# Optimization experiments

Measured on AMD Instinct MI355X. Metric: run time of the kernel, lower is better.

Reference implementation:

```python
import jax, jax.numpy as jnp
import numpy as np


def setup_inputs() -> dict:
    key = jax.random.key(0)
    k1, k2, k3 = jax.random.split(key, 3)
    B, S, D = 8, 2048, 1024
    lstm_output = jax.random.normal(k1, (B, S, D), dtype=jnp.float32)
    W = jax.random.normal(k2, (D, D), dtype=jnp.float32) * (1.0 / np.sqrt(D))
    b = jax.random.normal(k3, (D,), dtype=jnp.float32) * 0.01
    return {"lstm_output": lstm_output, "W": W, "b": b}


def reference(lstm_output, W, b):
    # proj(x) = x @ W^T + b  (torch nn.Linear convention: W is [out, in])
    proj = jnp.einsum('bsd,ed->bse', lstm_output, W) + b          # [B,S,D]
    # scores[b,i,j] = x[b,i] . proj[b,j]
    attn_scores = jnp.einsum('bid,bjd->bij', lstm_output, proj)   # [B,S,S]
    attn_weights = jax.nn.softmax(attn_scores, axis=-1)           # [B,S,S]
    context_vector = jnp.einsum('bij,bjd->bid', attn_weights, lstm_output)
    return (context_vector, attn_weights)
```

## Files before the change

### kernel.cpp

```cpp
#include <hip/hip_runtime.h>


typedef _Float16 f16;
typedef _Float16 f16x8 __attribute__((ext_vector_type(8)));
typedef _Float16 f16x4 __attribute__((ext_vector_type(4)));
typedef float f32x4 __attribute__((ext_vector_type(4)));
typedef unsigned int u32;

#define AS1 __attribute__((address_space(1)))
#define AS3 __attribute__((address_space(3)))

static constexpr int Bb = 8, Ss = 2048, Dd = 1024;

__global__ __launch_bounds__(256) void split_cast_k(
    const float* __restrict__ in, f16* __restrict__ hi, f16* __restrict__ lo,
    size_t n4) {
  size_t i = (size_t)blockIdx.x * 256 + threadIdx.x;
  if (i >= n4) return;
  float4 v = ((const float4*)in)[i];
  f16x4 h, l;
  h[0] = (f16)v.x; l[0] = (f16)(v.x - (float)h[0]);
  h[1] = (f16)v.y; l[1] = (f16)(v.y - (float)h[1]);
  h[2] = (f16)v.z; l[2] = (f16)(v.z - (float)h[2]);
  h[3] = (f16)v.w; l[3] = (f16)(v.w - (float)h[3]);
  ((f16x4*)hi)[i] = h;
  ((f16x4*)lo)[i] = l;
}

__global__ __launch_bounds__(256) void cast_k(const float* __restrict__ in,
                                              f16* __restrict__ out,
                                              size_t n4) {
  size_t i = (size_t)blockIdx.x * 256 + threadIdx.x;
  if (i >= n4) return;
  float4 v = ((const float4*)in)[i];
  f16x4 h;
  h[0] = (f16)v.x; h[1] = (f16)v.y; h[2] = (f16)v.z; h[3] = (f16)v.w;
  ((f16x4*)out)[i] = h;
}

__global__ __launch_bounds__(256) void transpose_cast_k(
    const float* __restrict__ x, f16* __restrict__ xT) {
  __shared__ f16 tile[32][33];
  const int b = blockIdx.z;
  const int s0 = blockIdx.x * 32, d0 = blockIdx.y * 32;
  const int tx = threadIdx.x & 31, ty = threadIdx.x >> 5;
  const float* xb = x + (size_t)b * Ss * Dd;
#pragma unroll
  for (int r = 0; r < 32; r += 8)
    tile[ty + r][tx] = (f16)xb[(size_t)(s0 + ty + r) * Dd + d0 + tx];
  __syncthreads();
  f16* xTb = xT + (size_t)b * Dd * Ss;
#pragma unroll
  for (int r = 0; r < 32; r += 8)
    xTb[(size_t)(d0 + ty + r) * Ss + s0 + tx] = tile[tx][ty + r];
}

template <int PPW>
__device__ __forceinline__ void stage_tile(const f16* __restrict__ g,
                                           size_t ld, f16* lds, int wave,
                                           int lane) {
#pragma unroll
  for (int c = 0; c < PPW; ++c) {
    int panel = wave * PPW + c;
    const f16* gp =
        g + (size_t)(panel * 16 + (lane & 15)) * ld + (lane >> 4) * 8;
    AS3 u32* lp = (AS3 u32*)(lds + panel * 512);
    __builtin_amdgcn_global_load_lds((const AS1 u32*)gp, lp, 16, 0, 0);
  }
}

template <bool DUAL_A, bool OUT_F16>
__global__ __launch_bounds__(256, 2) void gemm_bt(
    const f16* __restrict__ A0, const f16* __restrict__ A1,
    const f16* __restrict__ B0, float* __restrict__ C, f16* __restrict__ Ch,
    const float* __restrict__ bias, int K, size_t ldc, size_t sA, size_t sB,
    size_t sC) {
  const int tid = threadIdx.x;
  const int wave = tid >> 6, lane = tid & 63;
  const size_t tn = (size_t)blockIdx.x * 256;
  const size_t tm = (size_t)blockIdx.y * 128;
  const int b = blockIdx.z;

  constexpr int STAGE = (DUAL_A ? 4 : 3) * 4096;
  constexpr int BOFF = DUAL_A ? 8192 : 4096;
  __shared__ f16 smem[2 * STAGE];

  const f16* Ah = A0 + (size_t)b * sA + tm * (size_t)K;
  const f16* Al = DUAL_A ? (A1 + (size_t)b * sA + tm * (size_t)K) : nullptr;
  const f16* Bp = B0 + (size_t)b * sB + tn * (size_t)K;

  const int pA = (wave >> 1) * 4;
  const int pB = (wave & 1) * 8;

  auto stage_all = [&](int k, f16* buf) {
    stage_tile<2>(Ah + k, K, buf, wave, lane);
    if constexpr (DUAL_A) stage_tile<2>(Al + k, K, buf + 4096, wave, lane);
    stage_tile<4>(Bp + k, K, buf + BOFF, wave, lane);
  };

  f32x4 acc[4][8] = {};

  stage_all(0, smem);
  const int nIter = K / 32;
  for (int it = 0; it < nIter; ++it) {
    f16* cur = smem + (it & 1) * STAGE;
    f16* nxt = smem + ((it + 1) & 1) * STAGE;
    __syncthreads();
    if (it + 1 < nIter) stage_all((it + 1) * 32, nxt);
    f16x8 ah[4], al[4];
#pragma unroll
    for (int i = 0; i < 4; ++i) {
      ah[i] = *(const f16x8*)&cur[(pA + i) * 512 + lane * 8];
      if constexpr (DUAL_A)
        al[i] = *(const f16x8*)&cur[4096 + (pA + i) * 512 + lane * 8];
    }
#pragma unroll
    for (int j = 0; j < 8; ++j) {
      f16x8 bf = *(const f16x8*)&cur[BOFF + (pB + j) * 512 + lane * 8];
#pragma unroll
      for (int i = 0; i < 4; ++i) {
        acc[i][j] =
            __builtin_amdgcn_mfma_f32_16x16x32_f16(ah[i], bf, acc[i][j], 0, 0, 0);
        if constexpr (DUAL_A)
          acc[i][j] = __builtin_amdgcn_mfma_f32_16x16x32_f16(al[i], bf,
                                                             acc[i][j], 0, 0, 0);
      }
    }
  }

  const int wm = pA * 16, wn = pB * 16;
#pragma unroll
  for (int i = 0; i < 4; ++i) {
    size_t row0 = tm + wm + i * 16 + ((lane >> 4) << 2);
#pragma unroll
    for (int j = 0; j < 8; ++j) {
      size_t col = tn + wn + j * 16 + (lane & 15);
      float bj = bias ? bias[col] : 0.f;
#pragma unroll
      for (int r = 0; r < 4; ++r) {
        float v = acc[i][j][r] + bj;
        size_t off = (size_t)b * sC + (row0 + r) * ldc + col;
        if constexpr (OUT_F16)
          Ch[off] = (f16)v;
        else
          C[off] = v;
      }
    }
  }
}

__global__ __launch_bounds__(256) void softmax_k(float* __restrict__ sc,
                                                 f16* __restrict__ wh) {
  const size_t row = blockIdx.x;
  float* p = sc + row * 2048;
  f16* w = wh + row * 2048;
  const int t = threadIdx.x;
  float4 v0 = ((const float4*)p)[t];
  float4 v1 = ((const float4*)p)[256 + t];
  float m = fmaxf(fmaxf(fmaxf(v0.x, v0.y), fmaxf(v0.z, v0.w)),
                  fmaxf(fmaxf(v1.x, v1.y), fmaxf(v1.z, v1.w)));
#pragma unroll
  for (int o = 32; o; o >>= 1) m = fmaxf(m, __shfl_xor(m, o, 64));
  __shared__ float red[4];
  if ((t & 63) == 0) red[t >> 6] = m;
  __syncthreads();
  m = fmaxf(fmaxf(red[0], red[1]), fmaxf(red[2], red[3]));
  v0.x = __expf(v0.x - m);
  v0.y = __expf(v0.y - m);
  v0.z = __expf(v0.z - m);
  v0.w = __expf(v0.w - m);
  v1.x = __expf(v1.x - m);
  v1.y = __expf(v1.y - m);
  v1.z = __expf(v1.z - m);
  v1.w = __expf(v1.w - m);
  float s = v0.x + v0.y + v0.z + v0.w + v1.x + v1.y + v1.z + v1.w;
#pragma unroll
  for (int o = 32; o; o >>= 1) s += __shfl_xor(s, o, 64);
  __shared__ float red2[4];
  if ((t & 63) == 0) red2[t >> 6] = s;
  __syncthreads();
  s = red2[0] + red2[1] + red2[2] + red2[3];
  float inv = 1.0f / s;
  v0.x *= inv; v0.y *= inv; v0.z *= inv; v0.w *= inv;
  v1.x *= inv; v1.y *= inv; v1.z *= inv; v1.w *= inv;
  ((float4*)p)[t] = v0;
  ((float4*)p)[256 + t] = v1;
  f16x4 h0, h1;
  h0[0] = (f16)v0.x; h0[1] = (f16)v0.y; h0[2] = (f16)v0.z; h0[3] = (f16)v0.w;
  h1[0] = (f16)v1.x; h1[1] = (f16)v1.y; h1[2] = (f16)v1.z; h1[3] = (f16)v1.w;
  ((f16x4*)w)[t] = h0;
  ((f16x4*)w)[256 + t] = h1;
}

extern "C" void kernel_launch(void* const* d_in, const int* in_sizes, int n_in,
                              void* d_out, int out_size, void* d_ws,
                              size_t ws_size, hipStream_t stream) {
  (void)in_sizes; (void)n_in; (void)out_size; (void)ws_size;
  const float* x = (const float*)d_in[0];
  const float* W = (const float*)d_in[1];
  const float* bias = (const float*)d_in[2];
  float* ctx = (float*)d_out;
  float* scores = (float*)d_out + (size_t)Bb * Ss * Dd;

  const size_t nBSD = (size_t)Bb * Ss * Dd;
  const size_t nDD = (size_t)Dd * Dd;

  f16* p = (f16*)d_ws;
  f16* x_hi = p; p += nBSD;
  f16* x_lo = p; p += nBSD;
  f16* xT   = p; p += nBSD;
  f16* W_hi = p; p += nDD;
  f16* p_hi = p; p += nBSD;
  f16* attnw = x_hi;

  split_cast_k<<<(unsigned)(nBSD / 4 / 256), 256, 0, stream>>>(x, x_hi, x_lo,
                                                               nBSD / 4);
  cast_k<<<(unsigned)(nDD / 4 / 256), 256, 0, stream>>>(W, W_hi, nDD / 4);
  transpose_cast_k<<<dim3(Ss / 32, Dd / 32, Bb), 256, 0, stream>>>(x, xT);

  gemm_bt<true, true><<<dim3(Dd / 256, (Bb * Ss) / 128, 1), 256, 0, stream>>>(
      x_hi, x_lo, W_hi, nullptr, p_hi, bias, Dd, (size_t)Dd, 0, 0, 0);

  gemm_bt<true, false><<<dim3(Ss / 256, Ss / 128, Bb), 256, 0, stream>>>(
      x_hi, x_lo, p_hi, scores, nullptr, nullptr, Dd, (size_t)Ss,
      (size_t)Ss * Dd, (size_t)Ss * Dd, (size_t)Ss * Ss);

  softmax_k<<<Bb * Ss, 256, 0, stream>>>(scores, attnw);

  gemm_bt<false, false><<<dim3(Dd / 256, Ss / 128, Bb), 256, 0, stream>>>(
      attnw, nullptr, xT, ctx, nullptr, nullptr, Ss, (size_t)Dd,
      (size_t)Ss * Ss, (size_t)Dd * Ss, (size_t)Ss * Dd);
}
```

Measured before the change: 631.2 us.

## Enlarge GEMM tiles to 256x256 with 8 waves and triple-buffered LDS pipeline

The GEMM kernel now runs 512 threads on a 256x256 output tile. A three-stage LDS ring is filled asynchronously, and explicit vmcnt waits let loads run two iterations ahead while only a single barrier is used per iteration. MFMA sections are wrapped in raised wave priority. The aim is to improve reuse and hide global load latency, at the cost of large dynamic LDS (up to 144KB), which limits occupancy to one block per CU and may leave fewer blocks to fill the machine.

```diff
diff --git a/kernel.cpp b/kernel.cpp
--- a/kernel.cpp
+++ b/kernel.cpp
@@ -70,53 +70,68 @@
 }
 
 template <bool DUAL_A, bool OUT_F16>
-__global__ __launch_bounds__(256, 2) void gemm_bt(
+__global__ __launch_bounds__(512, 2) void gemm_bt(
     const f16* __restrict__ A0, const f16* __restrict__ A1,
     const f16* __restrict__ B0, float* __restrict__ C, f16* __restrict__ Ch,
     const float* __restrict__ bias, int K, size_t ldc, size_t sA, size_t sB,
     size_t sC) {
+  extern __shared__ f16 smem[];
   const int tid = threadIdx.x;
   const int wave = tid >> 6, lane = tid & 63;
   const size_t tn = (size_t)blockIdx.x * 256;
-  const size_t tm = (size_t)blockIdx.y * 128;
+  const size_t tm = (size_t)blockIdx.y * 256;
   const int b = blockIdx.z;
 
-  constexpr int STAGE = (DUAL_A ? 4 : 3) * 4096;
-  constexpr int BOFF = DUAL_A ? 8192 : 4096;
-  __shared__ f16 smem[2 * STAGE];
+  constexpr int STAGE = (DUAL_A ? 3 : 2) * 8192;
+  constexpr int BOFF = DUAL_A ? 16384 : 8192;
 
   const f16* Ah = A0 + (size_t)b * sA + tm * (size_t)K;
   const f16* Al = DUAL_A ? (A1 + (size_t)b * sA + tm * (size_t)K) : nullptr;
   const f16* Bp = B0 + (size_t)b * sB + tn * (size_t)K;
 
-  const int pA = (wave >> 1) * 4;
-  const int pB = (wave & 1) * 8;
+  const int wr = wave >> 1, wc = wave & 1;
+  const int pA = wr * 4;
+  const int pB = wc * 8;
+
+  f16* b0 = smem;
+  f16* b1 = smem + STAGE;
+  f16* b2 = smem + 2 * STAGE;
 
   auto stage_all = [&](int k, f16* buf) {
     stage_tile<2>(Ah + k, K, buf, wave, lane);
-    if constexpr (DUAL_A) stage_tile<2>(Al + k, K, buf + 4096, wave, lane);
-    stage_tile<4>(Bp + k, K, buf + BOFF, wave, lane);
+    if constexpr (DUAL_A) stage_tile<2>(Al + k, K, buf + 8192, wave, lane);
+    stage_tile<2>(Bp + k, K, buf + BOFF, wave, lane);
   };
 
   f32x4 acc[4][8] = {};
 
-  stage_all(0, smem);
   const int nIter = K / 32;
+  stage_all(0, b0);
+  stage_all(32, b1);
   for (int it = 0; it < nIter; ++it) {
-    f16* cur = smem + (it & 1) * STAGE;
-    f16* nxt = smem + ((it + 1) & 1) * STAGE;
-    __syncthreads();
-    if (it + 1 < nIter) stage_all((it + 1) * 32, nxt);
+    if (it < nIter - 1) {
+      if constexpr (DUAL_A)
+        asm volatile("s_waitcnt vmcnt(6)" ::: "memory");
+      else
+        asm volatile("s_waitcnt vmcnt(4)" ::: "memory");
+    } else {
+      asm volatile("s_waitcnt vmcnt(0)" ::: "memory");
+    }
+    __builtin_amdgcn_s_barrier();
+    asm volatile("" ::: "memory");
+    if (it + 2 < nIter) stage_all((it + 2) * 32, b2);
+
     f16x8 ah[4], al[4];
 #pragma unroll
     for (int i = 0; i < 4; ++i) {
-      ah[i] = *(const f16x8*)&cur[(pA + i) * 512 + lane * 8];
+      ah[i] = *(const f16x8*)&b0[(pA + i) * 512 + lane * 8];
       if constexpr (DUAL_A)
-        al[i] = *(const f16x8*)&cur[4096 + (pA + i) * 512 + lane * 8];
-    }
+        al[i] = *(const f16x8*)&b0[8192 + (pA + i) * 512 + lane * 8];
+    }
+    __builtin_amdgcn_s_setprio(1);
 #pragma unroll
     for (int j = 0; j < 8; ++j) {
-      f16x8 bf = *(const f16x8*)&cur[BOFF + (pB + j) * 512 + lane * 8];
+      f16x8 bf = *(const f16x8*)&b0[BOFF + (pB + j) * 512 + lane * 8];
 #pragma unroll
       for (int i = 0; i < 4; ++i) {
         acc[i][j] =
@@ -126,9 +141,11 @@
                                                              acc[i][j], 0, 0, 0);
       }
     }
-  }
-
-  const int wm = pA * 16, wn = pB * 16;
+    __builtin_amdgcn_s_setprio(0);
+    f16* t = b0; b0 = b1; b1 = b2; b2 = t;
+  }
+
+  const int wm = wr * 64, wn = wc * 128;
 #pragma unroll
   for (int i = 0; i < 4; ++i) {
     size_t row0 = tm + wm + i * 16 + ((lane >> 4) << 2);
@@ -213,21 +230,37 @@
   f16* p_hi = p; p += nBSD;
   f16* attnw = x_hi;
 
+  static bool attr_done = false;
+  if (!attr_done) {
+    hipFuncSetAttribute(reinterpret_cast<const void*>(&gemm_bt<true, true>),
+                        hipFuncAttributeMaxDynamicSharedMemorySize, 147456);
+    hipFuncSetAttribute(reinterpret_cast<const void*>(&gemm_bt<true, false>),
+                        hipFuncAttributeMaxDynamicSharedMemorySize, 147456);
+    hipFuncSetAttribute(reinterpret_cast<const void*>(&gemm_bt<false, false>),
+                        hipFuncAttributeMaxDynamicSharedMemorySize, 147456);
+    attr_done = true;
+  }
+  constexpr unsigned LDS_DUAL = 3u * 24576u * 2u;
+  constexpr unsigned LDS_SINGLE = 3u * 16384u * 2u;
+
   split_cast_k<<<(unsigned)(nBSD / 4 / 256), 256, 0, stream>>>(x, x_hi, x_lo,
                                                                nBSD / 4);
   cast_k<<<(unsigned)(nDD / 4 / 256), 256, 0, stream>>>(W, W_hi, nDD / 4);
   transpose_cast_k<<<dim3(Ss / 32, Dd / 32, Bb), 256, 0, stream>>>(x, xT);
 
-  gemm_bt<true, true><<<dim3(Dd / 256, (Bb * Ss) / 128, 1), 256, 0, stream>>>(
-      x_hi, x_lo, W_hi, nullptr, p_hi, bias, Dd, (size_t)Dd, 0, 0, 0);
-
-  gemm_bt<true, false><<<dim3(Ss / 256, Ss / 128, Bb), 256, 0, stream>>>(
-      x_hi, x_lo, p_hi, scores, nullptr, nullptr, Dd, (size_t)Ss,
-      (size_t)Ss * Dd, (size_t)Ss * Dd, (size_t)Ss * Ss);
+  gemm_bt<true, true>
+      <<<dim3(Dd / 256, (Bb * Ss) / 256, 1), 512, LDS_DUAL, stream>>>(
+          x_hi, x_lo, W_hi, nullptr, p_hi, bias, Dd, (size_t)Dd, 0, 0, 0);
+
+  gemm_bt<true, false>
+      <<<dim3(Ss / 256, Ss / 256, Bb), 512, LDS_DUAL, stream>>>(
+          x_hi, x_lo, p_hi, scores, nullptr, nullptr, Dd, (size_t)Ss,
+          (size_t)Ss * Dd, (size_t)Ss * Dd, (size_t)Ss * Ss);
 
   softmax_k<<<Bb * Ss, 256, 0, stream>>>(scores, attnw);
 
-  gemm_bt<false, false><<<dim3(Dd / 256, Ss / 128, Bb), 256, 0, stream>>>(
-      attnw, nullptr, xT, ctx, nullptr, nullptr, Ss, (size_t)Dd,
-      (size_t)Ss * Ss, (size_t)Dd * Ss, (size_t)Ss * Dd);
-}
+  gemm_bt<false, false>
+      <<<dim3(Dd / 256, Ss / 256, Bb), 512, LDS_SINGLE, stream>>>(
+          attnw, nullptr, xT, ctx, nullptr, nullptr, Ss, (size_t)Dd,
+          (size_t)Ss * Ss, (size_t)Dd * Ss, (size_t)Ss * Dd);
+}
```

After: 577.1 us. -8.6%, faster.
